# Kernel tuning notes

Measured on AMD Instinct MI355X. Metric: run time of the kernel, lower is better.

The kernel has to match this reference:

```python
import jax, jax.numpy as jnp
import numpy as np

HIDDEN = 256
B, SQ, SKV = 8, 2048, 2048
SCALE = float(np.sqrt(HIDDEN / 2.0))  # module uses sqrt(hidden_dim/2)


def setup_inputs() -> dict:
    key = jax.random.key(0)
    ks = jax.random.split(key, 9)
    s = 1.0 / np.sqrt(HIDDEN)
    return {
        "query": jax.random.normal(ks[0], (B, SQ, HIDDEN), jnp.float32),
        "key": jax.random.normal(ks[1], (B, SKV, HIDDEN), jnp.float32),
        "value": jax.random.normal(ks[2], (B, SKV, HIDDEN), jnp.float32),
        "Wq": jax.random.uniform(ks[3], (HIDDEN, HIDDEN), jnp.float32, -s, s),
        "bq": jax.random.uniform(ks[4], (HIDDEN,), jnp.float32, -s, s),
        "Wk": jax.random.uniform(ks[5], (HIDDEN, HIDDEN), jnp.float32, -s, s),
        "bk": jax.random.uniform(ks[6], (HIDDEN,), jnp.float32, -s, s),
        "Wv": jax.random.uniform(ks[7], (HIDDEN, HIDDEN), jnp.float32, -s, s),
        "bv": jax.random.uniform(ks[8], (HIDDEN,), jnp.float32, -s, s),
    }


def reference(query, key, value, Wq, bq, Wk, bk, Wv, bv):
    # Linear projections (torch Linear: x @ W.T + b)
    Q = jnp.einsum('bsd,ed->bse', query, Wq) + bq  # [B,SQ,H]
    K = jnp.einsum('bsd,ed->bse', key, Wk) + bk    # [B,SKV,H]
    V = jnp.einsum('bsd,ed->bse', value, Wv) + bv  # [B,SKV,H]
    scores = jnp.einsum('bqd,bkd->bqk', Q, K) / SCALE  # [B,SQ,SKV]
    weights = jax.nn.softmax(scores, axis=-1)
    return jnp.einsum('bqk,bkd->bqd', weights, V)  # [B,SQ,H]
```

## Files before the change

kernel.cpp:

```cpp
#include <hip/hip_runtime.h>

#define HID 256
#define NB 8
#define SQL 2048
#define SKV 2048
#define SPLIT 4
#define KPB (SKV / SPLIT)
#define KVB 32
#define NT (KPB / KVB)
#define NROW (NB * SQL)

typedef __attribute__((ext_vector_type(8))) short bf16x8;
typedef __attribute__((ext_vector_type(4))) float f32x4;
typedef __attribute__((ext_vector_type(16))) float f32x16;

static __device__ __forceinline__ unsigned short f2bf(float x) {
  union { float f; unsigned int u; } v; v.f = x;
  unsigned int r = v.u + 0x7FFFu + ((v.u >> 16) & 1u);
  return (unsigned short)(r >> 16);
}

__global__ void wconv_kernel(const float* __restrict__ Wq, const float* __restrict__ Wk,
                             const float* __restrict__ Wv, unsigned short* __restrict__ out) {
  int i = blockIdx.x * blockDim.x + threadIdx.x;
  if (i >= 3 * HID * HID) return;
  const float* src = (i < HID * HID) ? Wq : (i < 2 * HID * HID ? Wk : Wv);
  out[i] = f2bf(src[i & (HID * HID - 1)]);
}

__global__ __launch_bounds__(512, 4) void proj_kernel(
    const float* __restrict__ query, const float* __restrict__ key, const float* __restrict__ value,
    const unsigned short* __restrict__ Wb,
    const float* __restrict__ bq, const float* __restrict__ bk, const float* __restrict__ bv,
    unsigned short* __restrict__ Qb, unsigned short* __restrict__ Kb, unsigned short* __restrict__ Vtb) {
  __shared__ __align__(16) char wl[65536];
  int tid = threadIdx.x;
  int wave = tid >> 6, lane = tid & 63, lr = lane & 15, lg = lane >> 4;
  int blk = blockIdx.x;
  int mat = blk >> 8;
  int rem = blk & 255;
  int b = rem >> 5;
  int rt = (rem >> 1) & 15;
  int et = rem & 1;

  const float* X = (mat == 0) ? query : (mat == 1 ? key : value);
  const float* bias = (mat == 0) ? bq : (mat == 1 ? bk : bv);
  const char* Wsrc = (const char*)(Wb + mat * HID * HID + et * 128 * HID);

#pragma unroll
  for (int i = 0; i < 8; i++) {
    int c = i * 512 + tid;
    int e = c >> 5;
    int glo = e * 512 + (((c & 31) ^ (e & 7)) << 4);
    __builtin_amdgcn_global_load_lds(
        (const __attribute__((address_space(1))) unsigned int*)(Wsrc + glo),
        (__attribute__((address_space(3))) unsigned int*)(wl + c * 16), 16, 0, 0);
  }

  int row_a = rt * 128 + wave * 16 + lr;
  const float* xrow = X + ((size_t)(b * SQL + row_a)) * HID;
  bf16x8 af[8];
#pragma unroll
  for (int s = 0; s < 8; s++) {
    const float4* p = (const float4*)(xrow + s * 32 + lg * 8);
    float4 x0 = p[0], x1 = p[1];
    bf16x8 a;
    a[0] = (short)f2bf(x0.x); a[1] = (short)f2bf(x0.y); a[2] = (short)f2bf(x0.z); a[3] = (short)f2bf(x0.w);
    a[4] = (short)f2bf(x1.x); a[5] = (short)f2bf(x1.y); a[6] = (short)f2bf(x1.z); a[7] = (short)f2bf(x1.w);
    af[s] = a;
  }
  __syncthreads();

  int row_c = rt * 128 + wave * 16 + lg * 4;
#pragma unroll
  for (int eo = 0; eo < 8; eo++) {
    f32x4 acc = (f32x4){0.f, 0.f, 0.f, 0.f};
    int eL = eo * 16 + lr;
#pragma unroll
    for (int sl = 0; sl < 8; sl++) {
      bf16x8 bfr = *(const bf16x8*)(wl + eL * 512 + (((sl * 4 + lg) ^ (eL & 7)) << 4));
      acc = __builtin_amdgcn_mfma_f32_16x16x32_bf16(af[sl], bfr, acc, 0, 0, 0);
    }
    int e = et * 128 + eo * 16 + lr;
    float bv_ = bias[e];
    if (mat < 2) {
      unsigned short* dst = (mat == 0 ? Qb : Kb) + (size_t)(b * SQL) * HID;
#pragma unroll
      for (int i = 0; i < 4; i++)
        dst[(size_t)(row_c + i) * HID + e] = f2bf(acc[i] + bv_);
    } else {
      ushort4 v;
      v.x = f2bf(acc[0] + bv_); v.y = f2bf(acc[1] + bv_);
      v.z = f2bf(acc[2] + bv_); v.w = f2bf(acc[3] + bv_);
      *(ushort4*)(Vtb + ((size_t)(b * HID + e)) * SKV + row_c) = v;
    }
  }
}

__global__ __launch_bounds__(256, 2) void attn_kernel(
    const unsigned short* __restrict__ Qb, const unsigned short* __restrict__ Kb,
    const unsigned short* __restrict__ Vtb, unsigned short* __restrict__ Op,
    float* __restrict__ Ml) {
  __shared__ __align__(16) char KA[16384];
  __shared__ __align__(16) char KB[16384];
  __shared__ __align__(16) char VA[16384];
  __shared__ __align__(16) char VB[16384];
  int tid = threadIdx.x;
  int wave = tid >> 6, lane = tid & 63, l31 = lane & 31, h = lane >> 5;
  int bid = (blockIdx.x & 7) * 64 + (blockIdx.x >> 3);
  int b = bid >> 6, s = (bid >> 4) & 3, qt = bid & 15;
  int qrow0 = qt * 128 + wave * 32;
  int k0 = s * KPB;

  const char* Kc0 = (const char*)(Kb + (size_t)b * SKV * HID) + (size_t)k0 * (HID * 2);
  const char* Vc0 = (const char*)(Vtb + (size_t)b * HID * SKV) + (size_t)k0 * 2;

  int offK[4], offV[4];
#pragma unroll
  for (int i = 0; i < 4; i++) {
    int g = i * 256 + tid;
    int r = g >> 5, c = g & 31;
    int gr = (c & 24) | ((c ^ (r & 7)) & 7);
    offK[i] = r * 512 + gr * 16;
    int r2 = g >> 3, gp = g & 7;
    int pre = gp ^ (r2 & 7);
    int d = 2 * r2 + (pre >> 2), cc = pre & 3;
    offV[i] = d * (SKV * 2) + cc * 16;
  }

  auto stage = [&](int t, char* kdst, char* vdst) {
    const char* Ksrc = Kc0 + t * (KVB * HID * 2);
    const char* Vsrc = Vc0 + t * (KVB * 2);
#pragma unroll
    for (int i = 0; i < 4; i++)
      __builtin_amdgcn_global_load_lds(
          (const __attribute__((address_space(1))) unsigned int*)(Ksrc + offK[i]),
          (__attribute__((address_space(3))) unsigned int*)(kdst + (i * 256 + tid) * 16),
          16, 0, 0);
#pragma unroll
    for (int i = 0; i < 4; i++)
      __builtin_amdgcn_global_load_lds(
          (const __attribute__((address_space(1))) unsigned int*)(Vsrc + offV[i]),
          (__attribute__((address_space(3))) unsigned int*)(vdst + (i * 256 + tid) * 16),
          16, 0, 0);
  };

  bf16x8 qf[16];
  {
    const unsigned short* qrow = Qb + ((size_t)(b * SQL + qrow0 + l31)) * HID + h * 8;
#pragma unroll
    for (int ks = 0; ks < 16; ks++) qf[ks] = *(const bf16x8*)(qrow + ks * 16);
  }

  f32x16 acc[8];
#pragma unroll
  for (int dt = 0; dt < 8; dt++)
#pragma unroll
    for (int j = 0; j < 16; j++) acc[dt][j] = 0.f;

  float m = -1e30f, l = 0.f;
  const float kC = 1.44269504088896341f / 11.3137084989847604f;

  auto step = [&](const char* kb, const char* vb) {
    f32x16 p;
#pragma unroll
    for (int j = 0; j < 16; j++) p[j] = 0.f;
    __builtin_amdgcn_s_setprio(1);
#pragma unroll
    for (int ks = 0; ks < 16; ks++) {
      int gr0 = ks * 2 + h;
      int gr = (gr0 & 24) | ((gr0 ^ (l31 & 7)) & 7);
      bf16x8 kf = *(const bf16x8*)(kb + l31 * 512 + gr * 16);
      p = __builtin_amdgcn_mfma_f32_32x32x16_bf16(kf, qf[ks], p, 0, 0, 0);
    }
    __builtin_amdgcn_s_setprio(0);

    float tmax = p[0];
#pragma unroll
    for (int j = 1; j < 16; j++) tmax = fmaxf(tmax, p[j]);
    tmax = fmaxf(tmax, __shfl_xor(tmax, 32, 64));
    float msc = tmax * kC;
    if (!__all(msc <= m + 8.0f)) {
      float mn = fmaxf(m, msc);
      float al = exp2f(m - mn);
      l *= al;
      m = mn;
#pragma unroll
      for (int r = 0; r < 16; r++) {
        int qp = (r & 3) + 8 * (r >> 2) + 4 * h;
        float ar = __shfl(al, qp, 64);
#pragma unroll
        for (int dt = 0; dt < 8; dt++) acc[dt][r] *= ar;
      }
    }
#pragma unroll
    for (int j = 0; j < 16; j++) p[j] = exp2f(fmaf(p[j], kC, -m));
    float ts = 0.f;
#pragma unroll
    for (int j = 0; j < 16; j++) ts += p[j];
    ts += __shfl_xor(ts, 32, 64);
    l += ts;

#pragma unroll
    for (int k2 = 0; k2 < 2; k2++) {
      unsigned P0, P1, P2, P3;
      asm("v_cvt_pk_bf16_f32 %0, %1, %2" : "=v"(P0) : "v"(p[k2 * 8 + 0]), "v"(p[k2 * 8 + 1]));
      asm("v_cvt_pk_bf16_f32 %0, %1, %2" : "=v"(P1) : "v"(p[k2 * 8 + 2]), "v"(p[k2 * 8 + 3]));
      asm("v_cvt_pk_bf16_f32 %0, %1, %2" : "=v"(P2) : "v"(p[k2 * 8 + 4]), "v"(p[k2 * 8 + 5]));
      asm("v_cvt_pk_bf16_f32 %0, %1, %2" : "=v"(P3) : "v"(p[k2 * 8 + 6]), "v"(p[k2 * 8 + 7]));
      asm("v_permlane32_swap_b32 %0, %1" : "+v"(P0), "+v"(P2));
      asm("v_permlane32_swap_b32 %0, %1" : "+v"(P1), "+v"(P3));
      union { unsigned u[4]; bf16x8 v; } pa;
      pa.u[0] = P0; pa.u[1] = P1; pa.u[2] = P2; pa.u[3] = P3;
      __builtin_amdgcn_s_setprio(1);
#pragma unroll
      for (int dt = 0; dt < 8; dt++) {
        int d = dt * 32 + l31;
        int gp = ((d & 1) * 4 + k2 * 2 + h) ^ ((d >> 1) & 7);
        bf16x8 vf = *(const bf16x8*)(vb + (d >> 1) * 128 + gp * 16);
        acc[dt] = __builtin_amdgcn_mfma_f32_32x32x16_bf16(pa.v, vf, acc[dt], 0, 0, 0);
      }
      __builtin_amdgcn_s_setprio(0);
    }
  };

  stage(0, KA, VA);
  for (int it = 0; it < 8; ++it) {
    stage(it * 2 + 1, KB, VB);
    asm volatile("s_waitcnt vmcnt(8)" ::: "memory");
    __builtin_amdgcn_s_barrier();
    __builtin_amdgcn_sched_barrier(0);
    step(KA, VA);
    __builtin_amdgcn_s_barrier();
    stage((it * 2 + 2) & 15, KA, VA);
    asm volatile("s_waitcnt vmcnt(8)" ::: "memory");
    __builtin_amdgcn_s_barrier();
    __builtin_amdgcn_sched_barrier(0);
    step(KB, VB);
    __builtin_amdgcn_s_barrier();
  }

  if (h == 0) {
    size_t row = (size_t)b * SQL + qrow0 + l31;
    float2 ml; ml.x = m; ml.y = l;
    *(float2*)(Ml + ((size_t)s * NROW + row) * 2) = ml;
  }
#pragma unroll
  for (int r = 0; r < 16; r++) {
    int qp = (r & 3) + 8 * (r >> 2) + 4 * h;
    float linv = 1.0f / __shfl(l, qp, 64);
    size_t row = (size_t)b * SQL + qrow0 + qp;
#pragma unroll
    for (int dt = 0; dt < 8; dt++) {
      union { _Float16 hf; unsigned short u; } cv;
      cv.hf = (_Float16)(acc[dt][r] * linv);
      Op[((size_t)s * NROW + row) * HID + dt * 32 + l31] = cv.u;
    }
  }
}

__global__ __launch_bounds__(256) void comb_kernel(const unsigned short* __restrict__ Op,
                                                   const float* __restrict__ Ml,
                                                   float* __restrict__ out) {
  int idx = blockIdx.x * 256 + threadIdx.x;
  int row = idx >> 6;
  int d0 = (idx & 63) << 2;
  float mv[SPLIT], lv[SPLIT];
#pragma unroll
  for (int s = 0; s < SPLIT; s++) {
    float2 ml = *(const float2*)(Ml + ((size_t)s * NROW + row) * 2);
    mv[s] = ml.x; lv[s] = ml.y;
  }
  float M = mv[0];
#pragma unroll
  for (int s = 1; s < SPLIT; s++) M = fmaxf(M, mv[s]);
  float W = 0.f, w[SPLIT];
#pragma unroll
  for (int s = 0; s < SPLIT; s++) { w[s] = lv[s] * exp2f(mv[s] - M); W += w[s]; }
  float wi = 1.0f / W;
  float o0 = 0.f, o1 = 0.f, o2 = 0.f, o3 = 0.f;
#pragma unroll
  for (int s = 0; s < SPLIT; s++) {
    ushort4 u = *(const ushort4*)(Op + ((size_t)s * NROW + row) * HID + d0);
    union { unsigned short us; _Float16 hf; } c0, c1, c2, c3;
    c0.us = u.x; c1.us = u.y; c2.us = u.z; c3.us = u.w;
    o0 += w[s] * (float)c0.hf; o1 += w[s] * (float)c1.hf;
    o2 += w[s] * (float)c2.hf; o3 += w[s] * (float)c3.hf;
  }
  float4 res; res.x = o0 * wi; res.y = o1 * wi; res.z = o2 * wi; res.w = o3 * wi;
  *(float4*)(out + (size_t)row * HID + d0) = res;
}

extern "C" void kernel_launch(void* const* d_in, const int* in_sizes, int n_in,
                              void* d_out, int out_size, void* d_ws, size_t ws_size,
                              hipStream_t stream) {
  const float* query = (const float*)d_in[0];
  const float* key   = (const float*)d_in[1];
  const float* value = (const float*)d_in[2];
  const float* Wq = (const float*)d_in[3];
  const float* bq = (const float*)d_in[4];
  const float* Wk = (const float*)d_in[5];
  const float* bk = (const float*)d_in[6];
  const float* Wv = (const float*)d_in[7];
  const float* bv = (const float*)d_in[8];

  char* ws = (char*)d_ws;
  unsigned short* Wb  = (unsigned short*)ws;
  unsigned short* Qb  = (unsigned short*)(ws + 393216);
  unsigned short* Kb  = Qb + (size_t)NB * SQL * HID;
  unsigned short* Vtb = Kb + (size_t)NB * SKV * HID;
  unsigned short* Op  = Vtb + (size_t)NB * HID * SKV;
  float* Ml = (float*)(Op + (size_t)SPLIT * NROW * HID);

  hipLaunchKernelGGL(wconv_kernel, dim3(768), dim3(256), 0, stream, Wq, Wk, Wv, Wb);
  hipLaunchKernelGGL(proj_kernel, dim3(768), dim3(512), 0, stream,
                     query, key, value, Wb, bq, bk, bv, Qb, Kb, Vtb);
  hipLaunchKernelGGL(attn_kernel, dim3(512), dim3(256), 0, stream, Qb, Kb, Vtb, Op, Ml);
  hipLaunchKernelGGL(comb_kernel, dim3(4096), dim3(256), 0, stream, Op, Ml, (float*)d_out);
}
```

Measured before the change: 107.2 us.

## Simplify KV double-buffer loop, change LDS swizzles, split QK accumulation chain

Replaces the hand-unrolled ping-pong loop, with its explicit vmcnt waits and raw barriers, by a generic loop: prefetch the next tile, compute the current one, then __syncthreads. Changes the K and V LDS swizzle patterns to simpler XOR layouts, with V stored d-major at 64 bytes per row. Splits the QK^T MFMA chain into two independent accumulators to shorten the dependency chain, and drops the s_setprio hints. The goal is less bank conflict and address arithmetic and more MFMA ILP. The risk is that __syncthreads forces a full memory wait each iteration, which may expose load latency that the old partial vmcnt wait hid.

```diff
diff --git a/kernel.cpp b/kernel.cpp
--- a/kernel.cpp
+++ b/kernel.cpp
@@ -119,12 +119,10 @@
 #pragma unroll
   for (int i = 0; i < 4; i++) {
     int g = i * 256 + tid;
-    int r = g >> 5, c = g & 31;
-    int gr = (c & 24) | ((c ^ (r & 7)) & 7);
-    offK[i] = r * 512 + gr * 16;
-    int r2 = g >> 3, gp = g & 7;
-    int pre = gp ^ (r2 & 7);
-    int d = 2 * r2 + (pre >> 2), cc = pre & 3;
+    int ky = g >> 5, cs = g & 31;
+    offK[i] = ky * 512 + ((cs ^ ky) << 4);
+    int d = g >> 2, ccs = g & 3;
+    int cc = ccs ^ ((d >> 3) & 3);
     offV[i] = d * (SKV * 2) + cc * 16;
   }
 
@@ -162,18 +160,18 @@
   const float kC = 1.44269504088896341f / 11.3137084989847604f;
 
   auto step = [&](const char* kb, const char* vb) {
-    f32x16 p;
-#pragma unroll
-    for (int j = 0; j < 16; j++) p[j] = 0.f;
-    __builtin_amdgcn_s_setprio(1);
-#pragma unroll
-    for (int ks = 0; ks < 16; ks++) {
-      int gr0 = ks * 2 + h;
-      int gr = (gr0 & 24) | ((gr0 ^ (l31 & 7)) & 7);
-      bf16x8 kf = *(const bf16x8*)(kb + l31 * 512 + gr * 16);
-      p = __builtin_amdgcn_mfma_f32_32x32x16_bf16(kf, qf[ks], p, 0, 0, 0);
-    }
-    __builtin_amdgcn_s_setprio(0);
+    f32x16 p, p1;
+#pragma unroll
+    for (int j = 0; j < 16; j++) { p[j] = 0.f; p1[j] = 0.f; }
+#pragma unroll
+    for (int ks = 0; ks < 8; ks++) {
+      bf16x8 kf0 = *(const bf16x8*)(kb + l31 * 512 + (((ks * 2 + h) ^ l31) << 4));
+      bf16x8 kf1 = *(const bf16x8*)(kb + l31 * 512 + ((((ks + 8) * 2 + h) ^ l31) << 4));
+      p = __builtin_amdgcn_mfma_f32_32x32x16_bf16(kf0, qf[ks], p, 0, 0, 0);
+      p1 = __builtin_amdgcn_mfma_f32_32x32x16_bf16(kf1, qf[ks + 8], p1, 0, 0, 0);
+    }
+#pragma unroll
+    for (int j = 0; j < 16; j++) p[j] += p1[j];
 
     float tmax = p[0];
 #pragma unroll
@@ -212,32 +210,24 @@
       asm("v_permlane32_swap_b32 %0, %1" : "+v"(P1), "+v"(P3));
       union { unsigned u[4]; bf16x8 v; } pa;
       pa.u[0] = P0; pa.u[1] = P1; pa.u[2] = P2; pa.u[3] = P3;
-      __builtin_amdgcn_s_setprio(1);
+      int ccs_base = k2 * 2 + h;
 #pragma unroll
       for (int dt = 0; dt < 8; dt++) {
-        int d = dt * 32 + l31;
-        int gp = ((d & 1) * 4 + k2 * 2 + h) ^ ((d >> 1) & 7);
-        bf16x8 vf = *(const bf16x8*)(vb + (d >> 1) * 128 + gp * 16);
+        int ccs = (ccs_base ^ ((l31 >> 3) & 3)) & 3;
+        bf16x8 vf = *(const bf16x8*)(vb + dt * 2048 + l31 * 64 + ccs * 16);
         acc[dt] = __builtin_amdgcn_mfma_f32_32x32x16_bf16(pa.v, vf, acc[dt], 0, 0, 0);
       }
-      __builtin_amdgcn_s_setprio(0);
     }
   };
 
   stage(0, KA, VA);
-  for (int it = 0; it < 8; ++it) {
-    stage(it * 2 + 1, KB, VB);
-    asm volatile("s_waitcnt vmcnt(8)" ::: "memory");
-    __builtin_amdgcn_s_barrier();
-    __builtin_amdgcn_sched_barrier(0);
-    step(KA, VA);
-    __builtin_amdgcn_s_barrier();
-    stage((it * 2 + 2) & 15, KA, VA);
-    asm volatile("s_waitcnt vmcnt(8)" ::: "memory");
-    __builtin_amdgcn_s_barrier();
-    __builtin_amdgcn_sched_barrier(0);
-    step(KB, VB);
-    __builtin_amdgcn_s_barrier();
+  __syncthreads();
+  for (int t = 0; t < NT; t++) {
+    char* kb = (t & 1) ? KB : KA;
+    char* vb = (t & 1) ? VB : VA;
+    if (t + 1 < NT) stage(t + 1, (t & 1) ? KA : KB, (t & 1) ? VA : VB);
+    step(kb, vb);
+    __syncthreads();
   }
 
   if (h == 0) {
```

Result: no change. 108.0 us (+0.7%).
